# Optimization experiments

Measured on AMD Instinct MI355X. Metric: run time of the kernel, lower is better.

## Reference

```python
import jax, jax.numpy as jnp
import numpy as np

HIDDEN = 256
INPUT = 128
B, T = 256, 512
W_SCALE = 1.0 / np.sqrt(HIDDEN)  # matches PyTorch U(-1/sqrt(H), 1/sqrt(H)) magnitude


def setup_inputs() -> dict:
    key = jax.random.key(0)
    ks = jax.random.split(key, 5)
    x = jax.random.normal(ks[0], (B, T, INPUT), dtype=jnp.float32)
    W_ih = jax.random.normal(ks[1], (3 * HIDDEN, INPUT), dtype=jnp.float32) * W_SCALE
    W_hh = jax.random.normal(ks[2], (3 * HIDDEN, HIDDEN), dtype=jnp.float32) * W_SCALE
    b_ih = jax.random.normal(ks[3], (3 * HIDDEN,), dtype=jnp.float32) * W_SCALE
    b_hh = jax.random.normal(ks[4], (3 * HIDDEN,), dtype=jnp.float32) * W_SCALE
    return {"x": x, "W_ih": W_ih, "W_hh": W_hh, "b_ih": b_ih, "b_hh": b_hh}


def reference(x, W_ih, W_hh, b_ih, b_hh):
    # PyTorch GRU, gate order (r, z, n):
    #   r = sigmoid(W_ir x + b_ir + W_hr h + b_hr)
    #   z = sigmoid(W_iz x + b_iz + W_hz h + b_hz)
    #   n = tanh(W_in x + b_in + r * (W_hn h + b_hn))
    #   h' = (1 - z) * n + z * h
    Bsz = x.shape[0]
    H = W_hh.shape[1]
    # Precompute all input-to-gate projections once (big GEMM outside the scan).
    xg = jnp.einsum('bti,gi->btg', x, W_ih) + b_ih  # [B, T, 3H]

    def step(h, xg_t):
        hg = h @ W_hh.T + b_hh                      # [B, 3H]
        xr, xz, xn = jnp.split(xg_t, 3, axis=-1)
        hr, hz, hn = jnp.split(hg, 3, axis=-1)
        r = jax.nn.sigmoid(xr + hr)
        z = jax.nn.sigmoid(xz + hz)
        n = jnp.tanh(xn + r * hn)
        h_new = (1.0 - z) * n + z * h
        return h_new, h_new

    h0 = jnp.zeros((Bsz, H), dtype=x.dtype)
    _, hs = jax.lax.scan(step, h0, jnp.swapaxes(xg, 0, 1))  # hs: [T, B, H]
    return jnp.swapaxes(hs, 0, 1)                           # [B, T, H]
```

## Files before the change

### kernel.cpp

```cpp
#include <hip/hip_runtime.h>
#include <cstdint>
#include <cstddef>

typedef unsigned short u16;

#define HH 256
#define IIN 128
#define TT 512
#define G3 768

typedef __attribute__((ext_vector_type(8))) short bf16x8;
typedef __attribute__((ext_vector_type(4))) float f32x4;
typedef __attribute__((ext_vector_type(4))) int   i32x4;

__device__ __forceinline__ u16 f2bf(float f) {
    union { float f; uint32_t i; } c; c.f = f;
    uint32_t r = c.i + 0x7fffu + ((c.i >> 16) & 1u);
    return (u16)(r >> 16);
}
__device__ __forceinline__ float bf2f(u16 s) {
    union { uint32_t i; float f; } u; u.i = ((uint32_t)s) << 16; return u.f;
}
__device__ __forceinline__ float frcp(float x) { return __builtin_amdgcn_rcpf(x); }
__device__ __forceinline__ float sigm(float x) {
    float e = __expf(-fabsf(x));
    float s = frcp(1.f + e);
    return x >= 0.f ? s : 1.f - s;
}
__device__ __forceinline__ float tanh_f(float x) {
    float e = __expf(-2.f * fabsf(x));
    float t = (1.f - e) * frcp(1.f + e);
    return x >= 0.f ? t : -t;
}

#define LDS_BARRIER() asm volatile("s_waitcnt lgkmcnt(0)\n\ts_barrier" ::: "memory")

__global__ __launch_bounds__(256, 2) void xg_gemm(
    const float* __restrict__ x, const float* __restrict__ W_ih,
    const float* __restrict__ b_ih, const float* __restrict__ b_hh,
    u16* __restrict__ xg, int t0, int lt)
{
    __shared__ u16 xA[128 * 136];
    __shared__ u16 wB[128 * 136];
    __shared__ float biasS[128];
    const int tid = threadIdx.x;
    const int m0 = blockIdx.x * 128;
    const int TcM = (1 << lt) - 1;
    const int srow = tid >> 5, sc = (tid & 31) * 4;

    #pragma unroll
    for (int it = 0; it < 16; ++it) {
        int r = srow + it * 8;
        int row = m0 + r;
        int b = row >> lt;
        int t = t0 + (row & TcM);
        float4 xv = *(const float4*)(x + ((size_t)b * TT + t) * IIN + sc);
        ushort4 xs = { f2bf(xv.x), f2bf(xv.y), f2bf(xv.z), f2bf(xv.w) };
        *(ushort4*)&xA[r * 136 + sc] = xs;
    }

    const int lane = tid & 63, wv = tid >> 6;
    const int quad = lane >> 4, colL = lane & 15;

    #pragma unroll
    for (int nb = 0; nb < 2; ++nb) {
        const int n0 = blockIdx.y * 256 + nb * 128;
        if (nb) __syncthreads();
        #pragma unroll
        for (int it = 0; it < 16; ++it) {
            int r = srow + it * 8;
            float4 wv4 = *(const float4*)(W_ih + (size_t)(n0 + r) * IIN + sc);
            ushort4 ws4 = { f2bf(wv4.x), f2bf(wv4.y), f2bf(wv4.z), f2bf(wv4.w) };
            *(ushort4*)&wB[r * 136 + sc] = ws4;
        }
        if (tid < 128) {
            int n = n0 + tid;
            float bv = b_ih[n];
            if (n < 512) bv += b_hh[n];
            biasS[tid] = bv;
        }
        __syncthreads();

        f32x4 C[2][8] = {};
        #pragma unroll
        for (int kt = 0; kt < 4; ++kt) {
            bf16x8 A[2];
            #pragma unroll
            for (int i = 0; i < 2; ++i)
                A[i] = *(const bf16x8*)&xA[(wv * 32 + i * 16 + colL) * 136 + kt * 32 + quad * 8];
            #pragma unroll
            for (int nn = 0; nn < 8; ++nn) {
                bf16x8 Bf = *(const bf16x8*)&wB[(nn * 16 + colL) * 136 + kt * 32 + quad * 8];
                C[0][nn] = __builtin_amdgcn_mfma_f32_16x16x32_bf16(A[0], Bf, C[0][nn], 0, 0, 0);
                C[1][nn] = __builtin_amdgcn_mfma_f32_16x16x32_bf16(A[1], Bf, C[1][nn], 0, 0, 0);
            }
        }
        #pragma unroll
        for (int i = 0; i < 2; ++i)
            #pragma unroll
            for (int nn = 0; nn < 8; ++nn) {
                int c = nn * 16 + colL;
                float bv = biasS[c];
                #pragma unroll
                for (int r = 0; r < 4; ++r) {
                    int row = m0 + wv * 32 + i * 16 + quad * 4 + r;
                    xg[(size_t)row * G3 + n0 + c] = f2bf(C[i][nn][r] + bv);
                }
            }
    }
}

#define GRU_STEP(TC_, HBR_, HBW_, HQR_, HQW_, PR_, PZ_, PN_) do {              \
    f32x4 Cn[2] = {};                                                          \
    i32x4 Cr[2] = {}, Cz[2] = {};                                              \
    _Pragma("unroll")                                                          \
    for (int kt = 0; kt < 4; ++kt) {                                           \
        i32x4 Aq = *(const i32x4*)((const char*)(HQR_) + kt * 64 + quad * 16); \
        Cr[0] = __builtin_amdgcn_mfma_i32_16x16x64_i8(Aq, Br[0][kt], Cr[0], 0, 0, 0); \
        Cr[1] = __builtin_amdgcn_mfma_i32_16x16x64_i8(Aq, Br[1][kt], Cr[1], 0, 0, 0); \
        Cz[0] = __builtin_amdgcn_mfma_i32_16x16x64_i8(Aq, Bz[0][kt], Cz[0], 0, 0, 0); \
        Cz[1] = __builtin_amdgcn_mfma_i32_16x16x64_i8(Aq, Bz[1][kt], Cz[1], 0, 0, 0); \
    }                                                                          \
    _Pragma("unroll")                                                          \
    for (int kt = 0; kt < 8; ++kt) {                                           \
        bf16x8 A = *(const bf16x8*)&HBR_[kt * 32 + quad * 8];                  \
        Cn[0] = __builtin_amdgcn_mfma_f32_16x16x32_bf16(A, Bn[0][kt], Cn[0], 0, 0, 0); \
        Cn[1] = __builtin_amdgcn_mfma_f32_16x16x32_bf16(A, Bn[1][kt], Cn[1], 0, 0, 0); \
    }                                                                          \
    float dr = (float)(i16 ? Cr[1][0] : Cr[0][0]) * scR;                       \
    float dz = (float)(i16 ? Cz[1][0] : Cz[0][0]) * scZ;                       \
    float dn = i16 ? Cn[1][0] : Cn[0][0];                                      \
    float xr = PR_, xz = PZ_, xn = PN_;                                        \
    int t2 = (TC_) + 2; if (t2 > Tc - 1) t2 = Tc - 1;                          \
    const u16* p2 = xgb + (size_t)t2 * G3;                                     \
    PR_ = bf2f(p2[j]); PZ_ = bf2f(p2[256 + j]); PN_ = bf2f(p2[512 + j]);       \
    float r = sigm(xr + dr);                                                   \
    float z = sigm(xz + dz);                                                   \
    float n = tanh_f(xn + r * (dn + bhn));                                     \
    hreg = n + z * (hreg - n);                                                 \
    float hc = fminf(fmaxf(hreg, -1.f), 1.f);       \
    int hq8 = (int)rintf(hc * 127.f);                                          \
    if (lane < 32) {                                                           \
        HBW_[j] = f2bf(hreg);                                                  \
        ((char*)(HQW_))[j] = (char)hq8;                                        \
        outb[(size_t)(t0 + (TC_)) * HH + j] = hreg;                            \
    }                                                                          \
    LDS_BARRIER();                                                             \
} while (0)

__global__ __launch_bounds__(512, 1) void gru_seq(
    const float* __restrict__ W_hh, const float* __restrict__ b_hh,
    const u16* __restrict__ xg, float* __restrict__ out,
    float* __restrict__ hstate, int t0, int Tc)
{
    __shared__ __align__(16) u16 hBuf[2][HH];
    __shared__ __align__(16) int hqBuf[2][HH / 4];

    const int tid = threadIdx.x;
    const int lane = tid & 63, wv = tid >> 6;
    const int quad = lane >> 4, colL = lane & 15;
    const int i16 = quad & 1;
    const int j = wv * 32 + (lane & 31);
    const int b = blockIdx.x;

    bf16x8 Bn[2][8];
    #pragma unroll
    for (int i = 0; i < 2; ++i) {
        const size_t rowb = (size_t)(512 + wv * 32 + i * 16 + colL) * HH;
        #pragma unroll
        for (int kt = 0; kt < 8; ++kt) {
            float4 lo = *(const float4*)(W_hh + rowb + kt * 32 + quad * 8);
            float4 hi = *(const float4*)(W_hh + rowb + kt * 32 + quad * 8 + 4);
            union { bf16x8 v; u16 s[8]; } u;
            u.s[0] = f2bf(lo.x); u.s[1] = f2bf(lo.y);
            u.s[2] = f2bf(lo.z); u.s[3] = f2bf(lo.w);
            u.s[4] = f2bf(hi.x); u.s[5] = f2bf(hi.y);
            u.s[6] = f2bf(hi.z); u.s[7] = f2bf(hi.w);
            Bn[i][kt] = u.v;
        }
    }

    i32x4 Br[2][4], Bz[2][4];
    float scR = 0.f, scZ = 0.f;
    #pragma unroll
    for (int g = 0; g < 2; ++g) {
        #pragma unroll
        for (int i = 0; i < 2; ++i) {
            const float* wr = W_hh + (size_t)(g * 256 + wv * 32 + i * 16 + colL) * HH;
            float m = 0.f;
            #pragma unroll
            for (int kt = 0; kt < 4; ++kt)
                #pragma unroll
                for (int u4 = 0; u4 < 4; ++u4) {
                    float4 v = *(const float4*)(wr + kt * 64 + quad * 16 + u4 * 4);
                    m = fmaxf(m, fmaxf(fmaxf(fabsf(v.x), fabsf(v.y)),
                                       fmaxf(fabsf(v.z), fabsf(v.w))));
                }
            m = fmaxf(m, __shfl_xor(m, 16));
            m = fmaxf(m, __shfl_xor(m, 32));
            float inv = m > 1e-30f ? 127.f / m : 0.f;
            float sc  = m * (1.f / 16129.f);
            #pragma unroll
            for (int kt = 0; kt < 4; ++kt) {
                int pk[4];
                #pragma unroll
                for (int u4 = 0; u4 < 4; ++u4) {
                    float4 v = *(const float4*)(wr + kt * 64 + quad * 16 + u4 * 4);
                    int q0 = (int)rintf(fminf(fmaxf(v.x * inv, -127.f), 127.f));
                    int q1 = (int)rintf(fminf(fmaxf(v.y * inv, -127.f), 127.f));
                    int q2 = (int)rintf(fminf(fmaxf(v.z * inv, -127.f), 127.f));
                    int q3 = (int)rintf(fminf(fmaxf(v.w * inv, -127.f), 127.f));
                    pk[u4] = (q0 & 255) | ((q1 & 255) << 8) | ((q2 & 255) << 16) | (q3 << 24);
                }
                i32x4 t = { pk[0], pk[1], pk[2], pk[3] };
                if (g == 0) Br[i][kt] = t; else Bz[i][kt] = t;
            }
            if (i == i16) { if (g == 0) scR = sc; else scZ = sc; }
        }
    }

    float hreg = (t0 == 0) ? 0.f : hstate[b * HH + j];
    if (lane < 32) {
        hBuf[0][j] = f2bf(hreg);
        float hc = fminf(fmaxf(hreg, -1.f), 1.f);
        ((char*)hqBuf[0])[j] = (char)(int)rintf(hc * 127.f);
    }
    const float bhn = b_hh[512 + j];
    const u16* xgb = xg + (size_t)b * Tc * G3;
    float* outb = out + (size_t)b * TT * HH;

    float pr0 = bf2f(xgb[j]),      pz0 = bf2f(xgb[256 + j]),      pn0 = bf2f(xgb[512 + j]);
    float pr1 = bf2f(xgb[G3 + j]), pz1 = bf2f(xgb[G3 + 256 + j]), pn1 = bf2f(xgb[G3 + 512 + j]);
    __syncthreads();

    for (int tc = 0; tc < Tc; tc += 2) {
        GRU_STEP(tc,     hBuf[0], hBuf[1], hqBuf[0], hqBuf[1], pr0, pz0, pn0);
        GRU_STEP(tc + 1, hBuf[1], hBuf[0], hqBuf[1], hqBuf[0], pr1, pz1, pn1);
    }

    if (t0 + Tc < TT && lane < 32)
        hstate[b * HH + j] = hreg;
}

extern "C" void kernel_launch(void* const* d_in, const int* in_sizes, int n_in,
                              void* d_out, int out_size, void* d_ws, size_t ws_size,
                              hipStream_t stream) {
    const float* x    = (const float*)d_in[0];
    const float* W_ih = (const float*)d_in[1];
    const float* W_hh = (const float*)d_in[2];
    const float* b_ih = (const float*)d_in[3];
    const float* b_hh = (const float*)d_in[4];
    float* out = (float*)d_out;

    float* hstate = (float*)d_ws;
    u16* xg = (u16*)((char*)d_ws + 262144);
    size_t avail = ws_size > 262144 ? ws_size - 262144 : 0;

    int Tc = TT, lt = 9;
    while (Tc > 4 && (size_t)256 * Tc * G3 * 2 > avail) { Tc >>= 1; --lt; }

    for (int t0 = 0; t0 < TT; t0 += Tc) {
        xg_gemm<<<dim3(2 * Tc, G3 / 256), 256, 0, stream>>>(
            x, W_ih, b_ih, b_hh, xg, t0, lt);
        gru_seq<<<dim3(256), 512, 0, stream>>>(
            W_hh, b_hh, xg, out, hstate, t0, Tc);
    }
}
```

Before: 710.7 us.

## Keep W_ih tile resident in LDS and loop over eight row tiles per block

The input-projection GEMM now loads a 384-column slab of W_ih (three 128-col tiles) and its bias into LDS once per block. Each block then iterates over eight 128-row tiles of x, so the weight conversion and loading is amortized instead of repeated per row tile. The grid shrinks from 2*Tc by 3 blocks to Tc/4 by 2, with launch bounds lowered to one block per SIMD pair given the larger LDS footprint. This trades weight reloads for fewer blocks and less parallelism. The xg GEMM is likely a small part of total time next to the sequential GRU kernel.

Result: no change. 699.0 us (-1.7%).

```diff
diff --git a/kernel.cpp b/kernel.cpp
--- a/kernel.cpp
+++ b/kernel.cpp
@@ -35,78 +35,82 @@
 
 #define LDS_BARRIER() asm volatile("s_waitcnt lgkmcnt(0)\n\ts_barrier" ::: "memory")
 
-__global__ __launch_bounds__(256, 2) void xg_gemm(
+__global__ __launch_bounds__(256, 1) void xg_gemm(
     const float* __restrict__ x, const float* __restrict__ W_ih,
     const float* __restrict__ b_ih, const float* __restrict__ b_hh,
     u16* __restrict__ xg, int t0, int lt)
 {
     __shared__ u16 xA[128 * 136];
-    __shared__ u16 wB[128 * 136];
-    __shared__ float biasS[128];
+    __shared__ u16 wB[3][128 * 136];
+    __shared__ float biasS[384];
     const int tid = threadIdx.x;
-    const int m0 = blockIdx.x * 128;
     const int TcM = (1 << lt) - 1;
     const int srow = tid >> 5, sc = (tid & 31) * 4;
-
-    #pragma unroll
-    for (int it = 0; it < 16; ++it) {
-        int r = srow + it * 8;
-        int row = m0 + r;
-        int b = row >> lt;
-        int t = t0 + (row & TcM);
-        float4 xv = *(const float4*)(x + ((size_t)b * TT + t) * IIN + sc);
-        ushort4 xs = { f2bf(xv.x), f2bf(xv.y), f2bf(xv.z), f2bf(xv.w) };
-        *(ushort4*)&xA[r * 136 + sc] = xs;
-    }
-
     const int lane = tid & 63, wv = tid >> 6;
     const int quad = lane >> 4, colL = lane & 15;
 
     #pragma unroll
-    for (int nb = 0; nb < 2; ++nb) {
-        const int n0 = blockIdx.y * 256 + nb * 128;
-        if (nb) __syncthreads();
+    for (int w3 = 0; w3 < 3; ++w3) {
+        const int n0 = blockIdx.y * 384 + w3 * 128;
         #pragma unroll
         for (int it = 0; it < 16; ++it) {
             int r = srow + it * 8;
             float4 wv4 = *(const float4*)(W_ih + (size_t)(n0 + r) * IIN + sc);
             ushort4 ws4 = { f2bf(wv4.x), f2bf(wv4.y), f2bf(wv4.z), f2bf(wv4.w) };
-            *(ushort4*)&wB[r * 136 + sc] = ws4;
-        }
-        if (tid < 128) {
-            int n = n0 + tid;
-            float bv = b_ih[n];
-            if (n < 512) bv += b_hh[n];
-            biasS[tid] = bv;
+            *(ushort4*)&wB[w3][r * 136 + sc] = ws4;
+        }
+    }
+    for (int n = tid; n < 384; n += 256) {
+        int g = blockIdx.y * 384 + n;
+        float bv = b_ih[g];
+        if (g < 512) bv += b_hh[g];
+        biasS[n] = bv;
+    }
+
+    for (int xt = 0; xt < 8; ++xt) {
+        const int m0 = blockIdx.x * 1024 + xt * 128;
+        if (xt) __syncthreads();
+        #pragma unroll
+        for (int it = 0; it < 16; ++it) {
+            int r = srow + it * 8;
+            int row = m0 + r;
+            int b = row >> lt;
+            int t = t0 + (row & TcM);
+            float4 xv = *(const float4*)(x + ((size_t)b * TT + t) * IIN + sc);
+            ushort4 xs = { f2bf(xv.x), f2bf(xv.y), f2bf(xv.z), f2bf(xv.w) };
+            *(ushort4*)&xA[r * 136 + sc] = xs;
         }
         __syncthreads();
 
-        f32x4 C[2][8] = {};
-        #pragma unroll
-        for (int kt = 0; kt < 4; ++kt) {
-            bf16x8 A[2];
+        #pragma unroll
+        for (int w3 = 0; w3 < 3; ++w3) {
+            f32x4 C[2][8] = {};
+            #pragma unroll
+            for (int kt = 0; kt < 4; ++kt) {
+                bf16x8 A[2];
+                #pragma unroll
+                for (int i = 0; i < 2; ++i)
+                    A[i] = *(const bf16x8*)&xA[(wv * 32 + i * 16 + colL) * 136 + kt * 32 + quad * 8];
+                #pragma unroll
+                for (int nn = 0; nn < 8; ++nn) {
+                    bf16x8 Bf = *(const bf16x8*)&wB[w3][(nn * 16 + colL) * 136 + kt * 32 + quad * 8];
+                    C[0][nn] = __builtin_amdgcn_mfma_f32_16x16x32_bf16(A[0], Bf, C[0][nn], 0, 0, 0);
+                    C[1][nn] = __builtin_amdgcn_mfma_f32_16x16x32_bf16(A[1], Bf, C[1][nn], 0, 0, 0);
+                }
+            }
             #pragma unroll
             for (int i = 0; i < 2; ++i)
-                A[i] = *(const bf16x8*)&xA[(wv * 32 + i * 16 + colL) * 136 + kt * 32 + quad * 8];
-            #pragma unroll
-            for (int nn = 0; nn < 8; ++nn) {
-                bf16x8 Bf = *(const bf16x8*)&wB[(nn * 16 + colL) * 136 + kt * 32 + quad * 8];
-                C[0][nn] = __builtin_amdgcn_mfma_f32_16x16x32_bf16(A[0], Bf, C[0][nn], 0, 0, 0);
-                C[1][nn] = __builtin_amdgcn_mfma_f32_16x16x32_bf16(A[1], Bf, C[1][nn], 0, 0, 0);
-            }
-        }
-        #pragma unroll
-        for (int i = 0; i < 2; ++i)
-            #pragma unroll
-            for (int nn = 0; nn < 8; ++nn) {
-                int c = nn * 16 + colL;
-                float bv = biasS[c];
-                #pragma unroll
-                for (int r = 0; r < 4; ++r) {
-                    int row = m0 + wv * 32 + i * 16 + quad * 4 + r;
-                    xg[(size_t)row * G3 + n0 + c] = f2bf(C[i][nn][r] + bv);
-                }
-            }
+                #pragma unroll
+                for (int nn = 0; nn < 8; ++nn) {
+                    int cl = w3 * 128 + nn * 16 + colL;
+                    float bv = biasS[cl];
+                    #pragma unroll
+                    for (int r = 0; r < 4; ++r) {
+                        int row = m0 + wv * 32 + i * 16 + quad * 4 + r;
+                        xg[(size_t)row * G3 + blockIdx.y * 384 + cl] = f2bf(C[i][nn][r] + bv);
+                    }
+                }
+        }
     }
 }
 
@@ -260,7 +264,7 @@
     while (Tc > 4 && (size_t)256 * Tc * G3 * 2 > avail) { Tc >>= 1; --lt; }
 
     for (int t0 = 0; t0 < TT; t0 += Tc) {
-        xg_gemm<<<dim3(2 * Tc, G3 / 256), 256, 0, stream>>>(
+        xg_gemm<<<dim3(Tc / 4, 2), 256, 0, stream>>>(
             x, W_ih, b_ih, b_hh, xg, t0, lt);
         gru_seq<<<dim3(256), 512, 0, stream>>>(
             W_hh, b_hh, xg, out, hstate, t0, Tc);
```
